# Performance work log

Measured on AMD Instinct MI355X. Metric: run time of the kernel, lower is better.

## Reference

```python
import jax, jax.numpy as jnp
import numpy as np

N, E, FD, H, NG, LAT = 20000, 320000, 64, 4, 64, 512


def _gat(x, W, a_src, a_dst, b, src, dst):
    # x: [N, in]; W: [H*FD, in]; a_src/a_dst: [H, FD]; b: [H*FD]
    h = (x @ W.T).reshape(N, H, FD)
    s = jnp.sum(h * a_src, -1)   # [N, H]
    d = jnp.sum(h * a_dst, -1)   # [N, H]
    e = jax.nn.leaky_relu(s[src] + d[dst], negative_slope=0.2)  # [E', H]
    m = jax.ops.segment_max(e, dst, num_segments=N)
    ex = jnp.exp(e - m[dst])
    den = jax.ops.segment_sum(ex, dst, num_segments=N)
    alpha = ex / den[dst]                                        # [E', H]
    out = jax.ops.segment_sum(alpha[:, :, None] * h[src], dst, num_segments=N)
    return out.reshape(N, H * FD) + b


def setup_inputs() -> dict:
    key = jax.random.key(0)
    ks = jax.random.split(key, 24)
    inp = {}
    inp['street_feature'] = jax.random.normal(ks[0], (N, 128), jnp.float32)
    inp['building_feature'] = jax.random.normal(ks[1], (N, 5), jnp.float32)
    sm = jax.random.randint(ks[2], (N, 1), 0, 2).astype(jnp.float32)
    inp['street_mask'] = sm
    inp['building_mask'] = 1.0 - sm
    inp['edge_index'] = jax.random.randint(ks[3], (2, E), 0, N, dtype=jnp.int32)
    # batch: sorted graph ids covering all NG graphs (no empty segments)
    rest = jax.random.randint(ks[4], (N - NG,), 0, NG, dtype=jnp.int32)
    inp['batch'] = jnp.sort(jnp.concatenate([jnp.arange(NG, dtype=jnp.int32), rest]))

    def lin(k, o, i):
        s = 1.0 / np.sqrt(i)
        return jax.random.uniform(k, (o, i), jnp.float32, -s, s)

    inp['street_W'] = lin(ks[5], FD, 128); inp['street_b'] = jnp.zeros((FD,), jnp.float32)
    inp['building_W'] = lin(ks[6], FD, 5); inp['building_b'] = jnp.zeros((FD,), jnp.float32)
    inp['W1'] = lin(ks[7], H * FD, FD)
    inp['a_src1'] = jax.random.normal(ks[8], (H, FD), jnp.float32) * 0.1
    inp['a_dst1'] = jax.random.normal(ks[9], (H, FD), jnp.float32) * 0.1
    inp['b1'] = jnp.zeros((H * FD,), jnp.float32)
    inp['W2'] = lin(ks[10], H * FD, H * FD)
    inp['a_src2'] = jax.random.normal(ks[11], (H, FD), jnp.float32) * 0.1
    inp['a_dst2'] = jax.random.normal(ks[12], (H, FD), jnp.float32) * 0.1
    inp['b2'] = jnp.zeros((H * FD,), jnp.float32)
    inp['W3'] = lin(ks[13], H * FD, H * FD)
    inp['a_src3'] = jax.random.normal(ks[14], (H, FD), jnp.float32) * 0.1
    inp['a_dst3'] = jax.random.normal(ks[15], (H, FD), jnp.float32) * 0.1
    inp['b3'] = jnp.zeros((H * FD,), jnp.float32)
    agg_in = FD * (1 + H * 3)  # 832
    inp['agg_W'] = lin(ks[16], LAT, agg_in); inp['agg_b'] = jnp.zeros((LAT,), jnp.float32)
    inp['mu_W'] = lin(ks[17], LAT, LAT); inp['mu_b'] = jnp.zeros((LAT,), jnp.float32)
    inp['var_W'] = lin(ks[18], LAT, LAT); inp['var_b'] = jnp.zeros((LAT,), jnp.float32)
    return inp


def reference(street_feature, building_feature, street_mask, building_mask,
              edge_index, batch,
              street_W, street_b, building_W, building_b,
              W1, a_src1, a_dst1, b1, W2, a_src2, a_dst2, b2,
              W3, a_src3, a_dst3, b3, agg_W, agg_b, mu_W, mu_b, var_W, var_b):
    sf = jax.nn.relu(street_feature @ street_W.T + street_b)
    bf = jax.nn.relu(building_feature @ building_W.T + building_b)
    n0 = sf * street_mask + bf * building_mask  # [N, FD]
    # add self loops (PyG GATConv default)
    loop = jnp.arange(N, dtype=edge_index.dtype)
    src = jnp.concatenate([edge_index[0], loop])
    dst = jnp.concatenate([edge_index[1], loop])
    n1 = jax.nn.relu(_gat(n0, W1, a_src1, a_dst1, b1, src, dst))
    n2 = jax.nn.relu(_gat(n1, W2, a_src2, a_dst2, b2, src, dst))
    n3 = jax.nn.relu(_gat(n2, W3, a_src3, a_dst3, b3, src, dst))
    g0 = jax.ops.segment_max(n0, batch, num_segments=NG)
    g1 = jax.ops.segment_max(n1, batch, num_segments=NG)
    g2 = jax.ops.segment_max(n2, batch, num_segments=NG)
    g3 = jax.ops.segment_max(n3, batch, num_segments=NG)
    g = jnp.concatenate([g0, g1, g2, g3], axis=1)  # [NG, FD*(1+3H)]
    latent = g @ agg_W.T + agg_b
    mu = latent @ mu_W.T + mu_b
    log_var = latent @ var_W.T + var_b
    return (mu, log_var)
```

## Files before the change

kernel.cpp:

```cpp
#include <hip/hip_runtime.h>
#include <math.h>

#define NNODES 20000
#define NEDGES 320000
#define FDIM 64
#define NHEAD 4
#define NGR 64
#define LATD 512
#define HF 256
#define NEP (NEDGES + NNODES)
#define AGGIN 832
#define MPAD 20032

typedef float f32x4 __attribute__((ext_vector_type(4)));
typedef _Float16 f16x8 __attribute__((ext_vector_type(8)));
typedef unsigned short u16x8 __attribute__((ext_vector_type(8)));

__device__ inline unsigned short f2h(float f) {
    _Float16 h = (_Float16)f;
    unsigned short u;
    __builtin_memcpy(&u, &h, 2);
    return u;
}
__device__ inline float h2f(unsigned short u) {
    _Float16 h;
    __builtin_memcpy(&h, &u, 2);
    return (float)h;
}

#define EDGE_BLOCKS4 ((NEP + 1023) / 1024)
#define CONV_N (HF * FDIM + 2 * HF * HF)
#define CONV_BLOCKS ((CONV_N + 255) / 256)
#define ENC_BLOCKS (NNODES / 32)
#define GEMM_BLOCKS (NNODES / 32)
#define SLAB_BLOCKS (NNODES / 32)

__global__ void prep_kernel(
    const int* __restrict__ ei, int* __restrict__ cnt,
    const float* __restrict__ W1, const float* __restrict__ W2, const float* __restrict__ W3,
    unsigned short* __restrict__ W1f, unsigned short* __restrict__ W2f,
    unsigned short* __restrict__ W3f)
{
    if (blockIdx.x < EDGE_BLOCKS4) {
        int i0 = blockIdx.x * 1024 + threadIdx.x;
#pragma unroll
        for (int u = 0; u < 4; u++) {
            int i = i0 + u * 256;
            if (i < NEDGES) {
                atomicAdd(&cnt[ei[NEDGES + i]], 1);
            } else if (i < NEP) {
                atomicAdd(&cnt[i - NEDGES], 1);
            }
        }
    } else {
        int i = (blockIdx.x - EDGE_BLOCKS4) * 256 + threadIdx.x;
        const int n1 = HF * FDIM, n2 = HF * HF;
        const float* src; unsigned short* dst; int j;
        if (i < n1) { src = W1; dst = W1f; j = i; }
        else if (i < n1 + n2) { src = W2; dst = W2f; j = i - n1; }
        else if (i < n1 + 2 * n2) { src = W3; dst = W3f; j = i - n1 - n2; }
        else return;
        dst[j] = f2h(src[j]);
    }
}

__global__ __launch_bounds__(1024) void scan_deg(const int* __restrict__ deg, int* __restrict__ offs)
{
    __shared__ int wt[16];
    const int per = (NNODES + 1023) / 1024;
    int t = threadIdx.x, lane = t & 63, w = t >> 6;
    int start = t * per;
    int end = start + per; if (end > NNODES) end = NNODES;
    int s = 0;
    for (int i = start; i < end; i++) s += deg[i];
    int pref = s;
#pragma unroll
    for (int m = 1; m < 64; m <<= 1) {
        int v = __shfl_up(pref, m, 64);
        if (lane >= m) pref += v;
    }
    if (lane == 63) wt[w] = pref;
    __syncthreads();
    int wadd = 0;
    for (int i = 0; i < w; i++) wadd += wt[i];
    int acc = wadd + pref - s;
    for (int i = start; i < end; i++) { offs[i] = acc; acc += deg[i]; }
    if (t == 1023) offs[NNODES] = NEP;
}

__global__ void scatter_edges(const int* __restrict__ ei, const int* __restrict__ offs,
                              int* __restrict__ cnt2, int* __restrict__ csr_src)
{
    int i0 = blockIdx.x * 1024 + threadIdx.x;
    int sv[4], dv[4];
#pragma unroll
    for (int u = 0; u < 4; u++) {
        int i = i0 + u * 256;
        if (i < NEDGES) { sv[u] = ei[i]; dv[u] = ei[NEDGES + i]; }
        else if (i < NEP) { sv[u] = i - NEDGES; dv[u] = i - NEDGES; }
        else { sv[u] = -1; dv[u] = 0; }
    }
#pragma unroll
    for (int u = 0; u < 4; u++) {
        if (sv[u] >= 0) {
            int p = offs[dv[u]] + atomicAdd(&cnt2[dv[u]], 1);
            csr_src[p] = sv[u];
        }
    }
}

__global__ __launch_bounds__(256) void encode_n0(
    const float* __restrict__ sfeat, const float* __restrict__ bfeat,
    const float* __restrict__ smask, const float* __restrict__ bmask,
    const float* __restrict__ sW, const float* __restrict__ sb,
    const float* __restrict__ bW, const float* __restrict__ bb,
    const int* __restrict__ batch,
    unsigned short* __restrict__ x0, int* __restrict__ g)
{
    __shared__ float wlds[64 * 132];
    int t = threadIdx.x;
#pragma unroll
    for (int it = 0; it < 8; it++) {
        int idx = it * 256 + t;
        int f = idx >> 5, k4 = idx & 31;
        float4 v = *(const float4*)(sW + f * 128 + k4 * 4);
        *(float4*)(&wlds[f * 132 + k4 * 4]) = v;
    }
    __syncthreads();

    int lane = t & 63, wave = t >> 6;
    int nb = blockIdx.x * 32 + wave * 8;

    float acc[8];
#pragma unroll
    for (int i = 0; i < 8; i++) acc[i] = 0.f;

    const float* xbase = sfeat + (size_t)nb * 128;
    for (int k4 = 0; k4 < 32; k4++) {
        float4 wv = *(const float4*)(&wlds[lane * 132 + k4 * 4]);
#pragma unroll
        for (int i = 0; i < 8; i++) {
            float4 xv = *(const float4*)(xbase + i * 128 + k4 * 4);
            acc[i] += xv.x * wv.x + xv.y * wv.y + xv.z * wv.z + xv.w * wv.w;
        }
    }

    float bwr[5];
#pragma unroll
    for (int k = 0; k < 5; k++) bwr[k] = bW[lane * 5 + k];
    float sbv = sb[lane], bbv = bb[lane];

    int curb = batch[nb];
    float m = 0.f;
#pragma unroll
    for (int i = 0; i < 8; i++) {
        int node = nb + i;
        float accb = 0.f;
#pragma unroll
        for (int k = 0; k < 5; k++) accb += bfeat[node * 5 + k] * bwr[k];
        float sv = fmaxf(acc[i] + sbv, 0.f);
        float bv = fmaxf(accb + bbv, 0.f);
        float val = sv * smask[node] + bv * bmask[node];
        x0[(size_t)node * FDIM + lane] = f2h(val);
        int b = batch[node];
        if (b != curb) {
            atomicMax(&g[curb * AGGIN + lane], __float_as_int(m));
            m = 0.f; curb = b;
        }
        m = fmaxf(m, val);
    }
    atomicMax(&g[curb * AGGIN + lane], __float_as_int(m));
}

template <int K>
__global__ __launch_bounds__(256, 2) void gemm_attn_mfma(
    const unsigned short* __restrict__ xf, const unsigned short* __restrict__ Wf,
    const float* __restrict__ a_src, const float* __restrict__ a_dst,
    unsigned short* __restrict__ h, float* __restrict__ s, float* __restrict__ d,
    const int* __restrict__ batch, int* __restrict__ g, int slabcol)
{
    if (blockIdx.x >= GEMM_BLOCKS) {
        int f = threadIdx.x;
        int r0 = (blockIdx.x - GEMM_BLOCKS) * 32;
        int cur = batch[r0];
        float m = 0.f;
        for (int r = r0; r < r0 + 32; r += 4) {
            float v[4]; int bb[4];
#pragma unroll
            for (int i = 0; i < 4; i++) {
                v[i] = h2f(xf[(size_t)(r + i) * K + f]);
                bb[i] = batch[r + i];
            }
#pragma unroll
            for (int i = 0; i < 4; i++) {
                if (bb[i] != cur) {
                    atomicMax(&g[cur * AGGIN + slabcol + f], __float_as_int(m));
                    m = 0.f; cur = bb[i];
                }
                m = fmaxf(m, v[i]);
            }
        }
        atomicMax(&g[cur * AGGIN + slabcol + f], __float_as_int(m));
        return;
    }

    constexpr int NCHUNK = K / 64;
    int t = threadIdx.x, lane = t & 63, w = t >> 6;
    int colid = lane & 15, quad = lane >> 4;
    int nb = blockIdx.x * 32;

    f32x4 acc[2][4];
#pragma unroll
    for (int mt = 0; mt < 2; mt++)
#pragma unroll
        for (int nt = 0; nt < 4; nt++)
#pragma unroll
            for (int r = 0; r < 4; r++) acc[mt][nt][r] = 0.f;

#pragma unroll
    for (int c = 0; c < NCHUNK; c++) {
        const int kc = c * 64;
        f16x8 ah[2][2], bh[4][2];
#pragma unroll
        for (int half = 0; half < 2; half++) {
#pragma unroll
            for (int mt = 0; mt < 2; mt++) {
                size_t aoff = (size_t)(nb + mt * 16 + colid) * K + kc + half * 32 + quad * 8;
                ah[mt][half] = *(const f16x8*)&xf[aoff];
            }
#pragma unroll
            for (int nt = 0; nt < 4; nt++) {
                size_t boff = (size_t)(w * 64 + nt * 16 + colid) * K + kc + half * 32 + quad * 8;
                bh[nt][half] = *(const f16x8*)&Wf[boff];
            }
        }
        __builtin_amdgcn_sched_barrier(0);
#pragma unroll
        for (int half = 0; half < 2; half++)
#pragma unroll
            for (int mt = 0; mt < 2; mt++)
#pragma unroll
                for (int nt = 0; nt < 4; nt++)
                    acc[mt][nt] = __builtin_amdgcn_mfma_f32_16x16x32_f16(ah[mt][half], bh[nt][half], acc[mt][nt], 0, 0, 0);
    }

#pragma unroll
    for (int mt = 0; mt < 2; mt++) {
#pragma unroll
        for (int r = 0; r < 4; r++) {
            int node = nb + mt * 16 + quad * 4 + r;
#pragma unroll
            for (int nt = 0; nt < 4; nt++)
                h[(size_t)node * HF + w * 64 + nt * 16 + colid] = f2h(acc[mt][nt][r]);
        }
    }

    float as_r[4], ad_r[4];
#pragma unroll
    for (int nt = 0; nt < 4; nt++) {
        as_r[nt] = a_src[w * 64 + nt * 16 + colid];
        ad_r[nt] = a_dst[w * 64 + nt * 16 + colid];
    }
#pragma unroll
    for (int mt = 0; mt < 2; mt++) {
#pragma unroll
        for (int r = 0; r < 4; r++) {
            float ps = 0.f, pd = 0.f;
#pragma unroll
            for (int nt = 0; nt < 4; nt++) {
                ps += acc[mt][nt][r] * as_r[nt];
                pd += acc[mt][nt][r] * ad_r[nt];
            }
#pragma unroll
            for (int m = 1; m < 16; m <<= 1) {
                ps += __shfl_xor(ps, m, 64);
                pd += __shfl_xor(pd, m, 64);
            }
            if (colid == 0) {
                int node = nb + mt * 16 + quad * 4 + r;
                s[(size_t)node * NHEAD + w] = ps;
                d[(size_t)node * NHEAD + w] = pd;
            }
        }
    }
}

__global__ __launch_bounds__(256) void gat_aggr(
    const unsigned short* __restrict__ h, const float* __restrict__ s, const float* __restrict__ d,
    const int* __restrict__ offs, const int* __restrict__ csr_src,
    const float* __restrict__ bias, unsigned short* __restrict__ out)
{
    int t = threadIdx.x;
    int lane = t & 63;
    int wv = t >> 6;
    int node = blockIdx.x * 4 + wv;
    int eh = lane >> 5;
    int p = lane & 31;
    int hd2 = p >> 3;
    int f0 = p * 8;
    int lo = offs[node], hi = offs[node + 1];
    int deg = hi - lo;

    float a[8];
#pragma unroll
    for (int j = 0; j < 8; j++) a[j] = 0.f;
    float inv;

    if (deg <= 64) {
        int slot = lane >> 2, hd = lane & 3;
        float dn = d[(size_t)node * NHEAD + hd];
        float ev[4];
        int sv[4];
#pragma unroll
        for (int c = 0; c < 4; c++) {
            int k = c * 16 + slot;
            float e = -3.402823466e38f;
            int src = 0;
            if (k < deg) {
                src = csr_src[lo + k];
                float ee = s[(size_t)src * NHEAD + hd] + dn;
                e = fmaxf(ee, 0.2f * ee);
            }
            ev[c] = e; sv[c] = src;
        }
        float mx = fmaxf(fmaxf(ev[0], ev[1]), fmaxf(ev[2], ev[3]));
#pragma unroll
        for (int m = 4; m < 64; m <<= 1) mx = fmaxf(mx, __shfl_xor(mx, m, 64));
        float den = 0.f;
#pragma unroll
        for (int c = 0; c < 4; c++) {
            ev[c] = __expf(ev[c] - mx);
            den += ev[c];
        }
#pragma unroll
        for (int m = 4; m < 64; m <<= 1) den += __shfl_xor(den, m, 64);

        inv = 1.f / __shfl(den, hd2);

#pragma unroll
        for (int cb = 0; cb < 2; cb++) {
            if (cb * 32 >= deg) break;
            float ex[16]; int sr[16]; u16x8 hv[16];
#pragma unroll
            for (int cc = 0; cc < 2; cc++) {
                int c = cb * 2 + cc;
#pragma unroll
                for (int u = 0; u < 8; u++) {
                    int sl = (u * 2 + eh) * 4 + hd2;
                    ex[cc * 8 + u] = __shfl(ev[c], sl);
                    sr[cc * 8 + u] = __shfl(sv[c], sl);
                }
            }
#pragma unroll
            for (int u = 0; u < 16; u++)
                hv[u] = *(const u16x8*)(h + (size_t)sr[u] * HF + f0);
#pragma unroll
            for (int u = 0; u < 16; u++)
#pragma unroll
                for (int j = 0; j < 8; j++) a[j] += ex[u] * h2f(hv[u][j]);
        }
    } else {
        float dn2 = d[(size_t)node * NHEAD + hd2];
        float mx = -3.402823466e38f;
        for (int i = lo; i < hi; i++) {
            int src = csr_src[i];
            float e = s[(size_t)src * NHEAD + hd2] + dn2;
            e = fmaxf(e, 0.2f * e);
            mx = fmaxf(mx, e);
        }
        float den = 0.f;
        for (int i = lo + eh; i < hi; i += 2) {
            int src = csr_src[i];
            float e = s[(size_t)src * NHEAD + hd2] + dn2;
            e = fmaxf(e, 0.2f * e);
            float ex = __expf(e - mx);
            den += ex;
            u16x8 hv = *(const u16x8*)(h + (size_t)src * HF + f0);
#pragma unroll
            for (int j = 0; j < 8; j++) a[j] += ex * h2f(hv[j]);
        }
        den += __shfl_xor(den, 32, 64);
        inv = 1.f / den;
    }

#pragma unroll
    for (int j = 0; j < 8; j++) a[j] += __shfl_xor(a[j], 32, 64);

    if (eh == 0) {
        u16x8 ov;
#pragma unroll
        for (int j = 0; j < 8; j++)
            ov[j] = f2h(fmaxf(a[j] * inv + bias[f0 + j], 0.f));
        *(u16x8*)(out + (size_t)node * HF + f0) = ov;
    }
}

__global__ __launch_bounds__(256) void seg_max_slab_f16(
    const unsigned short* __restrict__ x, const int* __restrict__ batch,
    int* __restrict__ g, int coloff)
{
    int f = threadIdx.x;
    int r0 = blockIdx.x * 32;
    int cur = batch[r0];
    float m = 0.f;
    for (int r = r0; r < r0 + 32; r += 4) {
        float v[4]; int bb[4];
#pragma unroll
        for (int i = 0; i < 4; i++) {
            v[i] = h2f(x[(size_t)(r + i) * HF + f]);
            bb[i] = batch[r + i];
        }
#pragma unroll
        for (int i = 0; i < 4; i++) {
            if (bb[i] != cur) {
                atomicMax(&g[cur * AGGIN + coloff + f], __float_as_int(m));
                m = 0.f; cur = bb[i];
            }
            m = fmaxf(m, v[i]);
        }
    }
    atomicMax(&g[cur * AGGIN + coloff + f], __float_as_int(m));
}

__global__ __launch_bounds__(256) void mlp_latent(
    const float* __restrict__ g, const float* __restrict__ W, const float* __restrict__ b,
    float* __restrict__ latent)
{
    int idx = blockIdx.x * 256 + threadIdx.x;
    int r = idx >> 9, c = idx & 511;
    const float4* gv = (const float4*)(g + (size_t)r * AGGIN);
    const float4* wv = (const float4*)(W + (size_t)c * AGGIN);
    float acc = 0.f;
#pragma unroll 4
    for (int k = 0; k < AGGIN / 4; k++) {
        float4 a = gv[k], w = wv[k];
        acc += a.x * w.x + a.y * w.y + a.z * w.z + a.w * w.w;
    }
    latent[idx] = acc + b[c];
}

__global__ __launch_bounds__(256) void mlp_head(
    const float* __restrict__ latent,
    const float* __restrict__ muW, const float* __restrict__ mub,
    const float* __restrict__ vW, const float* __restrict__ vb,
    float* __restrict__ out)
{
    int idx = blockIdx.x * 256 + threadIdx.x;
    int half = idx >> 15;
    int j = idx & 32767;
    int r = j >> 9, c = j & 511;
    const float* W = half ? vW : muW;
    const float* bb = half ? vb : mub;
    const float4* lv = (const float4*)(latent + (size_t)r * LATD);
    const float4* wv = (const float4*)(W + (size_t)c * LATD);
    float acc = 0.f;
#pragma unroll 4
    for (int k = 0; k < LATD / 4; k++) {
        float4 a = lv[k], w = wv[k];
        acc += a.x * w.x + a.y * w.y + a.z * w.z + a.w * w.w;
    }
    out[idx] = acc + bb[c];
}

static inline size_t align16(size_t x) { return (x + 15) & ~(size_t)15; }

extern "C" void kernel_launch(void* const* d_in, const int* in_sizes, int n_in,
                              void* d_out, int out_size, void* d_ws, size_t ws_size,
                              hipStream_t stream)
{
    const float* sfeat = (const float*)d_in[0];
    const float* bfeat = (const float*)d_in[1];
    const float* smask = (const float*)d_in[2];
    const float* bmask = (const float*)d_in[3];
    const int*   ei    = (const int*)d_in[4];
    const int*   batch = (const int*)d_in[5];
    const float* sW = (const float*)d_in[6];
    const float* sb = (const float*)d_in[7];
    const float* bW = (const float*)d_in[8];
    const float* bb = (const float*)d_in[9];
    const float* W1 = (const float*)d_in[10];
    const float* as1 = (const float*)d_in[11];
    const float* ad1 = (const float*)d_in[12];
    const float* b1 = (const float*)d_in[13];
    const float* W2 = (const float*)d_in[14];
    const float* as2 = (const float*)d_in[15];
    const float* ad2 = (const float*)d_in[16];
    const float* b2 = (const float*)d_in[17];
    const float* W3 = (const float*)d_in[18];
    const float* as3 = (const float*)d_in[19];
    const float* ad3 = (const float*)d_in[20];
    const float* b3 = (const float*)d_in[21];
    const float* aggW = (const float*)d_in[22];
    const float* aggb = (const float*)d_in[23];
    const float* muW = (const float*)d_in[24];
    const float* mub = (const float*)d_in[25];
    const float* vW = (const float*)d_in[26];
    const float* vb = (const float*)d_in[27];
    float* out = (float*)d_out;

    char* ws = (char*)d_ws;
    size_t off = 0;
    unsigned short* h  = (unsigned short*)(ws + off); off = align16(off + (size_t)NNODES * HF * 2);
    unsigned short* x0 = (unsigned short*)(ws + off); off = align16(off + (size_t)MPAD * FDIM * 2);
    unsigned short* xA = (unsigned short*)(ws + off); off = align16(off + (size_t)MPAD * HF * 2);
    float* s  = (float*)(ws + off); off = align16(off + (size_t)NNODES * NHEAD * 4);
    float* d  = (float*)(ws + off); off = align16(off + (size_t)NNODES * NHEAD * 4);
    int* offs = (int*)(ws + off);   off = align16(off + (size_t)(NNODES + 1) * 4);
    size_t zstart = off;
    int* cnt  = (int*)(ws + off);   off = align16(off + (size_t)NNODES * 4);
    int* cnt2 = (int*)(ws + off);   off = align16(off + (size_t)NNODES * 4);
    float* g  = (float*)(ws + off); off = align16(off + (size_t)NGR * AGGIN * 4);
    size_t zbytes = off - zstart;
    int* csr  = (int*)(ws + off);   off = align16(off + (size_t)NEP * 4);
    float* lat = (float*)(ws + off); off = align16(off + (size_t)NGR * LATD * 4);
    unsigned short* W1f = (unsigned short*)(ws + off); off = align16(off + (size_t)HF * FDIM * 2);
    unsigned short* W2f = (unsigned short*)(ws + off); off = align16(off + (size_t)HF * HF * 2);
    unsigned short* W3f = (unsigned short*)(ws + off); off = align16(off + (size_t)HF * HF * 2);

    hipMemsetAsync(ws + zstart, 0, zbytes, stream);

    prep_kernel<<<EDGE_BLOCKS4 + CONV_BLOCKS, 256, 0, stream>>>(
        ei, cnt, W1, W2, W3, W1f, W2f, W3f);
    scan_deg<<<1, 1024, 0, stream>>>(cnt, offs);
    scatter_edges<<<EDGE_BLOCKS4, 256, 0, stream>>>(ei, offs, cnt2, csr);
    encode_n0<<<ENC_BLOCKS, 256, 0, stream>>>(
        sfeat, bfeat, smask, bmask, sW, sb, bW, bb, batch, x0, (int*)g);

    gemm_attn_mfma<FDIM><<<GEMM_BLOCKS, 256, 0, stream>>>(
        x0, W1f, as1, ad1, h, s, d, batch, (int*)g, -1);
    gat_aggr<<<NNODES / 4, 256, 0, stream>>>(h, s, d, offs, csr, b1, xA);

    gemm_attn_mfma<HF><<<GEMM_BLOCKS + SLAB_BLOCKS, 256, 0, stream>>>(
        xA, W2f, as2, ad2, h, s, d, batch, (int*)g, FDIM);
    gat_aggr<<<NNODES / 4, 256, 0, stream>>>(h, s, d, offs, csr, b2, xA);

    gemm_attn_mfma<HF><<<GEMM_BLOCKS + SLAB_BLOCKS, 256, 0, stream>>>(
        xA, W3f, as3, ad3, h, s, d, batch, (int*)g, FDIM + HF);
    gat_aggr<<<NNODES / 4, 256, 0, stream>>>(h, s, d, offs, csr, b3, xA);

    seg_max_slab_f16<<<SLAB_BLOCKS, 256, 0, stream>>>(xA, batch, (int*)g, FDIM + 2 * HF);

    mlp_latent<<<(NGR * LATD + 255) / 256, 256, 0, stream>>>(g, aggW, aggb, lat);
    mlp_head<<<(2 * NGR * LATD + 255) / 256, 256, 0, stream>>>(lat, muW, mub, vW, vb, out);
}
```

Baseline: 386.2 us.

## Fuse whole pipeline into one cooperative persistent kernel with grid syncs

```diff
diff --git a/kernel.cpp b/kernel.cpp
--- a/kernel.cpp
+++ b/kernel.cpp
@@ -1,5 +1,8 @@
 #include <hip/hip_runtime.h>
+#include <hip/hip_cooperative_groups.h>
 #include <math.h>
+
+namespace cg = cooperative_groups;
 
 #define NNODES 20000
 #define NEDGES 320000
@@ -12,104 +15,62 @@
 #define AGGIN 832
 #define MPAD 20032
 
-typedef float f32x4 __attribute__((ext_vector_type(4)));
-typedef _Float16 f16x8 __attribute__((ext_vector_type(8)));
-typedef unsigned short u16x8 __attribute__((ext_vector_type(8)));
-
-__device__ inline unsigned short f2h(float f) {
-    _Float16 h = (_Float16)f;
-    unsigned short u;
-    __builtin_memcpy(&u, &h, 2);
-    return u;
-}
-__device__ inline float h2f(unsigned short u) {
-    _Float16 h;
-    __builtin_memcpy(&h, &u, 2);
-    return (float)h;
-}
-
 #define EDGE_BLOCKS4 ((NEP + 1023) / 1024)
 #define CONV_N (HF * FDIM + 2 * HF * HF)
 #define CONV_BLOCKS ((CONV_N + 255) / 256)
 #define ENC_BLOCKS (NNODES / 32)
 #define GEMM_BLOCKS (NNODES / 32)
 #define SLAB_BLOCKS (NNODES / 32)
-
-__global__ void prep_kernel(
-    const int* __restrict__ ei, int* __restrict__ cnt,
+#define AGGR_BLOCKS (NNODES / 4)
+
+typedef float f32x4 __attribute__((ext_vector_type(4)));
+typedef _Float16 f16x8 __attribute__((ext_vector_type(8)));
+typedef unsigned short u16x8 __attribute__((ext_vector_type(8)));
+
+__device__ inline unsigned short f2h(float f) {
+    _Float16 h = (_Float16)f;
+    unsigned short u;
+    __builtin_memcpy(&u, &h, 2);
+    return u;
+}
+__device__ inline float h2f(unsigned short u) {
+    _Float16 h;
+    __builtin_memcpy(&h, &u, 2);
+    return (float)h;
+}
+
+
+__device__ __forceinline__ void count_body(int vb, int t,
+    const int* __restrict__ ei, int* __restrict__ cnt)
+{
+    int i0 = vb * 1024 + t;
+#pragma unroll
+    for (int u = 0; u < 4; u++) {
+        int i = i0 + u * 256;
+        if (i < NEDGES) {
+            atomicAdd(&cnt[ei[NEDGES + i]], 1);
+        } else if (i < NEP) {
+            atomicAdd(&cnt[i - NEDGES], 1);
+        }
+    }
+}
+
+__device__ __forceinline__ void convert_body(int vb, int t,
     const float* __restrict__ W1, const float* __restrict__ W2, const float* __restrict__ W3,
     unsigned short* __restrict__ W1f, unsigned short* __restrict__ W2f,
     unsigned short* __restrict__ W3f)
 {
-    if (blockIdx.x < EDGE_BLOCKS4) {
-        int i0 = blockIdx.x * 1024 + threadIdx.x;
-#pragma unroll
-        for (int u = 0; u < 4; u++) {
-            int i = i0 + u * 256;
-            if (i < NEDGES) {
-                atomicAdd(&cnt[ei[NEDGES + i]], 1);
-            } else if (i < NEP) {
-                atomicAdd(&cnt[i - NEDGES], 1);
-            }
-        }
-    } else {
-        int i = (blockIdx.x - EDGE_BLOCKS4) * 256 + threadIdx.x;
-        const int n1 = HF * FDIM, n2 = HF * HF;
-        const float* src; unsigned short* dst; int j;
-        if (i < n1) { src = W1; dst = W1f; j = i; }
-        else if (i < n1 + n2) { src = W2; dst = W2f; j = i - n1; }
-        else if (i < n1 + 2 * n2) { src = W3; dst = W3f; j = i - n1 - n2; }
-        else return;
-        dst[j] = f2h(src[j]);
-    }
-}
-
-__global__ __launch_bounds__(1024) void scan_deg(const int* __restrict__ deg, int* __restrict__ offs)
-{
-    __shared__ int wt[16];
-    const int per = (NNODES + 1023) / 1024;
-    int t = threadIdx.x, lane = t & 63, w = t >> 6;
-    int start = t * per;
-    int end = start + per; if (end > NNODES) end = NNODES;
-    int s = 0;
-    for (int i = start; i < end; i++) s += deg[i];
-    int pref = s;
-#pragma unroll
-    for (int m = 1; m < 64; m <<= 1) {
-        int v = __shfl_up(pref, m, 64);
-        if (lane >= m) pref += v;
-    }
-    if (lane == 63) wt[w] = pref;
-    __syncthreads();
-    int wadd = 0;
-    for (int i = 0; i < w; i++) wadd += wt[i];
-    int acc = wadd + pref - s;
-    for (int i = start; i < end; i++) { offs[i] = acc; acc += deg[i]; }
-    if (t == 1023) offs[NNODES] = NEP;
-}
-
-__global__ void scatter_edges(const int* __restrict__ ei, const int* __restrict__ offs,
-                              int* __restrict__ cnt2, int* __restrict__ csr_src)
-{
-    int i0 = blockIdx.x * 1024 + threadIdx.x;
-    int sv[4], dv[4];
-#pragma unroll
-    for (int u = 0; u < 4; u++) {
-        int i = i0 + u * 256;
-        if (i < NEDGES) { sv[u] = ei[i]; dv[u] = ei[NEDGES + i]; }
-        else if (i < NEP) { sv[u] = i - NEDGES; dv[u] = i - NEDGES; }
-        else { sv[u] = -1; dv[u] = 0; }
-    }
-#pragma unroll
-    for (int u = 0; u < 4; u++) {
-        if (sv[u] >= 0) {
-            int p = offs[dv[u]] + atomicAdd(&cnt2[dv[u]], 1);
-            csr_src[p] = sv[u];
-        }
-    }
-}
-
-__global__ __launch_bounds__(256) void encode_n0(
+    int i = vb * 256 + t;
+    const int n1 = HF * FDIM, n2 = HF * HF;
+    const float* src; unsigned short* dst; int j;
+    if (i < n1) { src = W1; dst = W1f; j = i; }
+    else if (i < n1 + n2) { src = W2; dst = W2f; j = i - n1; }
+    else if (i < n1 + 2 * n2) { src = W3; dst = W3f; j = i - n1 - n2; }
+    else return;
+    dst[j] = f2h(src[j]);
+}
+
+__device__ __forceinline__ void encode_body(int venc, int t, bool& wloaded, float* wlds,
     const float* __restrict__ sfeat, const float* __restrict__ bfeat,
     const float* __restrict__ smask, const float* __restrict__ bmask,
     const float* __restrict__ sW, const float* __restrict__ sb,
@@ -117,19 +78,20 @@
     const int* __restrict__ batch,
     unsigned short* __restrict__ x0, int* __restrict__ g)
 {
-    __shared__ float wlds[64 * 132];
-    int t = threadIdx.x;
-#pragma unroll
-    for (int it = 0; it < 8; it++) {
-        int idx = it * 256 + t;
-        int f = idx >> 5, k4 = idx & 31;
-        float4 v = *(const float4*)(sW + f * 128 + k4 * 4);
-        *(float4*)(&wlds[f * 132 + k4 * 4]) = v;
+    if (!wloaded) {
+#pragma unroll
+        for (int it = 0; it < 8; it++) {
+            int idx = it * 256 + t;
+            int f = idx >> 5, k4 = idx & 31;
+            float4 v = *(const float4*)(sW + f * 128 + k4 * 4);
+            *(float4*)(&wlds[f * 132 + k4 * 4]) = v;
+        }
+        wloaded = true;
     }
     __syncthreads();
 
     int lane = t & 63, wave = t >> 6;
-    int nb = blockIdx.x * 32 + wave * 8;
+    int nb = venc * 32 + wave * 8;
 
     float acc[8];
 #pragma unroll
@@ -172,42 +134,62 @@
     atomicMax(&g[curb * AGGIN + lane], __float_as_int(m));
 }
 
+__device__ __forceinline__ void scan_body(int t,
+    const int* __restrict__ deg, int* __restrict__ offs, int* wt)
+{
+    const int per = (NNODES + 255) / 256;
+    int lane = t & 63, w = t >> 6;
+    int start = t * per;
+    int end = start + per; if (end > NNODES) end = NNODES;
+    int s = 0;
+    for (int i = start; i < end; i++) s += deg[i];
+    int pref = s;
+#pragma unroll
+    for (int m = 1; m < 64; m <<= 1) {
+        int v = __shfl_up(pref, m, 64);
+        if (lane >= m) pref += v;
+    }
+    if (lane == 63) wt[w] = pref;
+    __syncthreads();
+    int wadd = 0;
+    for (int i = 0; i < w; i++) wadd += wt[i];
+    int acc = wadd + pref - s;
+    for (int i = start; i < end; i++) { offs[i] = acc; acc += deg[i]; }
+    if (t == 255) offs[NNODES] = NEP;
+}
+
+__device__ __forceinline__ void scatter_body(int vb, int t,
+    const int* __restrict__ ei, const int* __restrict__ offs,
+    int* __restrict__ cnt2, int* __restrict__ csr_src)
+{
+    int i0 = vb * 1024 + t;
+    int sv[4], dv[4];
+#pragma unroll
+    for (int u = 0; u < 4; u++) {
+        int i = i0 + u * 256;
+        if (i < NEDGES) { sv[u] = ei[i]; dv[u] = ei[NEDGES + i]; }
+        else if (i < NEP) { sv[u] = i - NEDGES; dv[u] = i - NEDGES; }
+        else { sv[u] = -1; dv[u] = 0; }
+    }
+#pragma unroll
+    for (int u = 0; u < 4; u++) {
+        if (sv[u] >= 0) {
+            int p = offs[dv[u]] + atomicAdd(&cnt2[dv[u]], 1);
+            csr_src[p] = sv[u];
+        }
+    }
+}
+
 template <int K>
-__global__ __launch_bounds__(256, 2) void gemm_attn_mfma(
+__device__ __forceinline__ void gemm_body(int vbg, int t,
     const unsigned short* __restrict__ xf, const unsigned short* __restrict__ Wf,
     const float* __restrict__ a_src, const float* __restrict__ a_dst,
-    unsigned short* __restrict__ h, float* __restrict__ s, float* __restrict__ d,
-    const int* __restrict__ batch, int* __restrict__ g, int slabcol)
-{
-    if (blockIdx.x >= GEMM_BLOCKS) {
-        int f = threadIdx.x;
-        int r0 = (blockIdx.x - GEMM_BLOCKS) * 32;
-        int cur = batch[r0];
-        float m = 0.f;
-        for (int r = r0; r < r0 + 32; r += 4) {
-            float v[4]; int bb[4];
-#pragma unroll
-            for (int i = 0; i < 4; i++) {
-                v[i] = h2f(xf[(size_t)(r + i) * K + f]);
-                bb[i] = batch[r + i];
-            }
-#pragma unroll
-            for (int i = 0; i < 4; i++) {
-                if (bb[i] != cur) {
-                    atomicMax(&g[cur * AGGIN + slabcol + f], __float_as_int(m));
-                    m = 0.f; cur = bb[i];
-                }
-                m = fmaxf(m, v[i]);
-            }
-        }
-        atomicMax(&g[cur * AGGIN + slabcol + f], __float_as_int(m));
-        return;
-    }
-
+    unsigned short* __restrict__ h, float* __restrict__ s, float* __restrict__ d)
+{
     constexpr int NCHUNK = K / 64;
-    int t = threadIdx.x, lane = t & 63, w = t >> 6;
+    int lane = t & 63, w = t >> 6;
     int colid = lane & 15, quad = lane >> 4;
-    int nb = blockIdx.x * 32;
+    int nb = vbg * 32;
 
     f32x4 acc[2][4];
 #pragma unroll
@@ -285,15 +267,14 @@
     }
 }
 
-__global__ __launch_bounds__(256) void gat_aggr(
+__device__ __forceinline__ void aggr_body(int vba, int t,
     const unsigned short* __restrict__ h, const float* __restrict__ s, const float* __restrict__ d,
     const int* __restrict__ offs, const int* __restrict__ csr_src,
     const float* __restrict__ bias, unsigned short* __restrict__ out)
 {
-    int t = threadIdx.x;
     int lane = t & 63;
     int wv = t >> 6;
-    int node = blockIdx.x * 4 + wv;
+    int node = vba * 4 + wv;
     int eh = lane >> 5;
     int p = lane & 31;
     int hd2 = p >> 3;
@@ -395,12 +376,12 @@
     }
 }
 
-__global__ __launch_bounds__(256) void seg_max_slab_f16(
+__device__ __forceinline__ void slab_body(int vbs, int t,
     const unsigned short* __restrict__ x, const int* __restrict__ batch,
     int* __restrict__ g, int coloff)
 {
-    int f = threadIdx.x;
-    int r0 = blockIdx.x * 32;
+    int f = t;
+    int r0 = vbs * 32;
     int cur = batch[r0];
     float m = 0.f;
     for (int r = r0; r < r0 + 32; r += 4) {
@@ -422,11 +403,11 @@
     atomicMax(&g[cur * AGGIN + coloff + f], __float_as_int(m));
 }
 
-__global__ __launch_bounds__(256) void mlp_latent(
+__device__ __forceinline__ void latent_body(int vb, int t,
     const float* __restrict__ g, const float* __restrict__ W, const float* __restrict__ b,
     float* __restrict__ latent)
 {
-    int idx = blockIdx.x * 256 + threadIdx.x;
+    int idx = vb * 256 + t;
     int r = idx >> 9, c = idx & 511;
     const float4* gv = (const float4*)(g + (size_t)r * AGGIN);
     const float4* wv = (const float4*)(W + (size_t)c * AGGIN);
@@ -439,18 +420,18 @@
     latent[idx] = acc + b[c];
 }
 
-__global__ __launch_bounds__(256) void mlp_head(
+__device__ __forceinline__ void head_body(int vb, int t,
     const float* __restrict__ latent,
     const float* __restrict__ muW, const float* __restrict__ mub,
-    const float* __restrict__ vW, const float* __restrict__ vb,
+    const float* __restrict__ vW, const float* __restrict__ vb_,
     float* __restrict__ out)
 {
-    int idx = blockIdx.x * 256 + threadIdx.x;
+    int idx = vb * 256 + t;
     int half = idx >> 15;
     int j = idx & 32767;
     int r = j >> 9, c = j & 511;
     const float* W = half ? vW : muW;
-    const float* bb = half ? vb : mub;
+    const float* bb = half ? vb_ : mub;
     const float4* lv = (const float4*)(latent + (size_t)r * LATD);
     const float4* wv = (const float4*)(W + (size_t)c * LATD);
     float acc = 0.f;
@@ -462,84 +443,255 @@
     out[idx] = acc + bb[c];
 }
 
+struct MegaParams {
+    const float *sfeat, *bfeat, *smask, *bmask;
+    const int *ei, *batch;
+    const float *sW, *sb, *bW, *bb;
+    const float *W1, *as1, *ad1, *b1;
+    const float *W2, *as2, *ad2, *b2;
+    const float *W3, *as3, *ad3, *b3;
+    const float *aggW, *aggb, *muW, *mub, *vW, *varb;
+    float *out;
+    unsigned short *h, *x0, *xA, *W1f, *W2f, *W3f;
+    float *s, *d, *g, *lat;
+    int *offs, *cnt, *cnt2, *csr, *gi;
+};
+
+__global__ __launch_bounds__(256, 2) void mega(MegaParams P)
+{
+    cg::grid_group grid = cg::this_grid();
+    __shared__ float wlds[64 * 132];
+    __shared__ int wt[4];
+    const int t = threadIdx.x;
+    const int bid = blockIdx.x;
+    const int G = gridDim.x;
+    bool wloaded = false;
+
+    for (int vb = bid; vb < EDGE_BLOCKS4 + CONV_BLOCKS + ENC_BLOCKS; vb += G) {
+        if (vb < EDGE_BLOCKS4)
+            count_body(vb, t, P.ei, P.cnt);
+        else if (vb < EDGE_BLOCKS4 + CONV_BLOCKS)
+            convert_body(vb - EDGE_BLOCKS4, t, P.W1, P.W2, P.W3, P.W1f, P.W2f, P.W3f);
+        else
+            encode_body(vb - (EDGE_BLOCKS4 + CONV_BLOCKS), t, wloaded, wlds,
+                        P.sfeat, P.bfeat, P.smask, P.bmask, P.sW, P.sb, P.bW, P.bb,
+                        P.batch, P.x0, P.gi);
+    }
+    grid.sync();
+
+    if (bid == G - 1) {
+        scan_body(t, P.cnt, P.offs, wt);
+    } else {
+        for (int vb = bid; vb < GEMM_BLOCKS; vb += G - 1)
+            gemm_body<FDIM>(vb, t, P.x0, P.W1f, P.as1, P.ad1, P.h, P.s, P.d);
+    }
+    grid.sync();
+
+    for (int vb = bid; vb < EDGE_BLOCKS4; vb += G)
+        scatter_body(vb, t, P.ei, P.offs, P.cnt2, P.csr);
+    grid.sync();
+
+    for (int vb = bid; vb < AGGR_BLOCKS; vb += G)
+        aggr_body(vb, t, P.h, P.s, P.d, P.offs, P.csr, P.b1, P.xA);
+    grid.sync();
+
+    for (int vb = bid; vb < GEMM_BLOCKS + SLAB_BLOCKS; vb += G) {
+        if (vb < GEMM_BLOCKS)
+            gemm_body<HF>(vb, t, P.xA, P.W2f, P.as2, P.ad2, P.h, P.s, P.d);
+        else
+            slab_body(vb - GEMM_BLOCKS, t, P.xA, P.batch, P.gi, FDIM);
+    }
+    grid.sync();
+
+    for (int vb = bid; vb < AGGR_BLOCKS; vb += G)
+        aggr_body(vb, t, P.h, P.s, P.d, P.offs, P.csr, P.b2, P.xA);
+    grid.sync();
+
+    for (int vb = bid; vb < GEMM_BLOCKS + SLAB_BLOCKS; vb += G) {
+        if (vb < GEMM_BLOCKS)
+            gemm_body<HF>(vb, t, P.xA, P.W3f, P.as3, P.ad3, P.h, P.s, P.d);
+        else
+            slab_body(vb - GEMM_BLOCKS, t, P.xA, P.batch, P.gi, FDIM + HF);
+    }
+    grid.sync();
+
+    for (int vb = bid; vb < AGGR_BLOCKS; vb += G)
+        aggr_body(vb, t, P.h, P.s, P.d, P.offs, P.csr, P.b3, P.xA);
+    grid.sync();
+
+    for (int vb = bid; vb < SLAB_BLOCKS; vb += G)
+        slab_body(vb, t, P.xA, P.batch, P.gi, FDIM + 2 * HF);
+    grid.sync();
+
+    for (int vb = bid; vb < (NGR * LATD) / 256; vb += G)
+        latent_body(vb, t, P.g, P.aggW, P.aggb, P.lat);
+    grid.sync();
+
+    for (int vb = bid; vb < (2 * NGR * LATD) / 256; vb += G)
+        head_body(vb, t, P.lat, P.muW, P.mub, P.vW, P.varb, P.out);
+}
+
+__global__ __launch_bounds__(256) void k_prep(MegaParams P)
+{
+    if ((int)blockIdx.x < EDGE_BLOCKS4)
+        count_body(blockIdx.x, threadIdx.x, P.ei, P.cnt);
+    else
+        convert_body(blockIdx.x - EDGE_BLOCKS4, threadIdx.x, P.W1, P.W2, P.W3,
+                     P.W1f, P.W2f, P.W3f);
+}
+
+__global__ __launch_bounds__(256) void k_scan(MegaParams P)
+{
+    __shared__ int wt[4];
+    scan_body(threadIdx.x, P.cnt, P.offs, wt);
+}
+
+__global__ __launch_bounds__(256) void k_scatter_encode(MegaParams P)
+{
+    __shared__ float wlds[64 * 132];
+    bool wloaded = false;
+    if ((int)blockIdx.x < EDGE_BLOCKS4)
+        scatter_body(blockIdx.x, threadIdx.x, P.ei, P.offs, P.cnt2, P.csr);
+    else
+        encode_body(blockIdx.x - EDGE_BLOCKS4, threadIdx.x, wloaded, wlds,
+                    P.sfeat, P.bfeat, P.smask, P.bmask, P.sW, P.sb, P.bW, P.bb,
+                    P.batch, P.x0, P.gi);
+}
+
+template <int K>
+__global__ __launch_bounds__(256, 2) void k_gemm(MegaParams P,
+    const unsigned short* xf, const unsigned short* Wf,
+    const float* a_src, const float* a_dst, int slabcol)
+{
+    if ((int)blockIdx.x >= GEMM_BLOCKS) {
+        slab_body(blockIdx.x - GEMM_BLOCKS, threadIdx.x, xf, P.batch, P.gi, slabcol);
+        return;
+    }
+    gemm_body<K>(blockIdx.x, threadIdx.x, xf, Wf, a_src, a_dst, P.h, P.s, P.d);
+}
+
+__global__ __launch_bounds__(256) void k_aggr(MegaParams P, const float* bias)
+{
+    aggr_body(blockIdx.x, threadIdx.x, P.h, P.s, P.d, P.offs, P.csr, bias, P.xA);
+}
+
+__global__ __launch_bounds__(256) void k_slab(MegaParams P, int coloff)
+{
+    slab_body(blockIdx.x, threadIdx.x, P.xA, P.batch, P.gi, coloff);
+}
+
+__global__ __launch_bounds__(256) void k_latent(MegaParams P)
+{
+    latent_body(blockIdx.x, threadIdx.x, P.g, P.aggW, P.aggb, P.lat);
+}
+
+__global__ __launch_bounds__(256) void k_head(MegaParams P)
+{
+    head_body(blockIdx.x, threadIdx.x, P.lat, P.muW, P.mub, P.vW, P.varb, P.out);
+}
+
 static inline size_t align16(size_t x) { return (x + 15) & ~(size_t)15; }
 
 extern "C" void kernel_launch(void* const* d_in, const int* in_sizes, int n_in,
                               void* d_out, int out_size, void* d_ws, size_t ws_size,
                               hipStream_t stream)
 {
-    const float* sfeat = (const float*)d_in[0];
-    const float* bfeat = (const float*)d_in[1];
-    const float* smask = (const float*)d_in[2];
-    const float* bmask = (const float*)d_in[3];
-    const int*   ei    = (const int*)d_in[4];
-    const int*   batch = (const int*)d_in[5];
-    const float* sW = (const float*)d_in[6];
-    const float* sb = (const float*)d_in[7];
-    const float* bW = (const float*)d_in[8];
-    const float* bb = (const float*)d_in[9];
-    const float* W1 = (const float*)d_in[10];
-    const float* as1 = (const float*)d_in[11];
-    const float* ad1 = (const float*)d_in[12];
-    const float* b1 = (const float*)d_in[13];
-    const float* W2 = (const float*)d_in[14];
-    const float* as2 = (const float*)d_in[15];
-    const float* ad2 = (const float*)d_in[16];
-    const float* b2 = (const float*)d_in[17];
-    const float* W3 = (const float*)d_in[18];
-    const float* as3 = (const float*)d_in[19];
-    const float* ad3 = (const float*)d_in[20];
-    const float* b3 = (const float*)d_in[21];
-    const float* aggW = (const float*)d_in[22];
-    const float* aggb = (const float*)d_in[23];
-    const float* muW = (const float*)d_in[24];
-    const float* mub = (const float*)d_in[25];
-    const float* vW = (const float*)d_in[26];
-    const float* vb = (const float*)d_in[27];
-    float* out = (float*)d_out;
+    MegaParams P;
+    P.sfeat = (const float*)d_in[0];
+    P.bfeat = (const float*)d_in[1];
+    P.smask = (const float*)d_in[2];
+    P.bmask = (const float*)d_in[3];
+    P.ei    = (const int*)d_in[4];
+    P.batch = (const int*)d_in[5];
+    P.sW = (const float*)d_in[6];
+    P.sb = (const float*)d_in[7];
+    P.bW = (const float*)d_in[8];
+    P.bb = (const float*)d_in[9];
+    P.W1 = (const float*)d_in[10];
+    P.as1 = (const float*)d_in[11];
+    P.ad1 = (const float*)d_in[12];
+    P.b1 = (const float*)d_in[13];
+    P.W2 = (const float*)d_in[14];
+    P.as2 = (const float*)d_in[15];
+    P.ad2 = (const float*)d_in[16];
+    P.b2 = (const float*)d_in[17];
+    P.W3 = (const float*)d_in[18];
+    P.as3 = (const float*)d_in[19];
+    P.ad3 = (const float*)d_in[20];
+    P.b3 = (const float*)d_in[21];
+    P.aggW = (const float*)d_in[22];
+    P.aggb = (const float*)d_in[23];
+    P.muW = (const float*)d_in[24];
+    P.mub = (const float*)d_in[25];
+    P.vW = (const float*)d_in[26];
+    P.varb = (const float*)d_in[27];
+    P.out = (float*)d_out;
 
     char* ws = (char*)d_ws;
     size_t off = 0;
-    unsigned short* h  = (unsigned short*)(ws + off); off = align16(off + (size_t)NNODES * HF * 2);
-    unsigned short* x0 = (unsigned short*)(ws + off); off = align16(off + (size_t)MPAD * FDIM * 2);
-    unsigned short* xA = (unsigned short*)(ws + off); off = align16(off + (size_t)MPAD * HF * 2);
-    float* s  = (float*)(ws + off); off = align16(off + (size_t)NNODES * NHEAD * 4);
-    float* d  = (float*)(ws + off); off = align16(off + (size_t)NNODES * NHEAD * 4);
-    int* offs = (int*)(ws + off);   off = align16(off + (size_t)(NNODES + 1) * 4);
+    P.h  = (unsigned short*)(ws + off); off = align16(off + (size_t)NNODES * HF * 2);
+    P.x0 = (unsigned short*)(ws + off); off = align16(off + (size_t)MPAD * FDIM * 2);
+    P.xA = (unsigned short*)(ws + off); off = align16(off + (size_t)MPAD * HF * 2);
+    P.s  = (float*)(ws + off); off = align16(off + (size_t)NNODES * NHEAD * 4);
+    P.d  = (float*)(ws + off); off = align16(off + (size_t)NNODES * NHEAD * 4);
+    P.offs = (int*)(ws + off); off = align16(off + (size_t)(NNODES + 1) * 4);
     size_t zstart = off;
-    int* cnt  = (int*)(ws + off);   off = align16(off + (size_t)NNODES * 4);
-    int* cnt2 = (int*)(ws + off);   off = align16(off + (size_t)NNODES * 4);
-    float* g  = (float*)(ws + off); off = align16(off + (size_t)NGR * AGGIN * 4);
+    P.cnt  = (int*)(ws + off); off = align16(off + (size_t)NNODES * 4);
+    P.cnt2 = (int*)(ws + off); off = align16(off + (size_t)NNODES * 4);
+    P.g    = (float*)(ws + off); off = align16(off + (size_t)NGR * AGGIN * 4);
     size_t zbytes = off - zstart;
-    int* csr  = (int*)(ws + off);   off = align16(off + (size_t)NEP * 4);
-    float* lat = (float*)(ws + off); off = align16(off + (size_t)NGR * LATD * 4);
-    unsigned short* W1f = (unsigned short*)(ws + off); off = align16(off + (size_t)HF * FDIM * 2);
-    unsigned short* W2f = (unsigned short*)(ws + off); off = align16(off + (size_t)HF * HF * 2);
-    unsigned short* W3f = (unsigned short*)(ws + off); off = align16(off + (size_t)HF * HF * 2);
+    P.csr = (int*)(ws + off); off = align16(off + (size_t)NEP * 4);
+    P.lat = (float*)(ws + off); off = align16(off + (size_t)NGR * LATD * 4);
+    P.W1f = (unsigned short*)(ws + off); off = align16(off + (size_t)HF * FDIM * 2);
+    P.W2f = (unsigned short*)(ws + off); off = align16(off + (size_t)HF * HF * 2);
+    P.W3f = (unsigned short*)(ws + off); off = align16(off + (size_t)HF * HF * 2);
+
+    P.gi = (int*)P.g;
 
     hipMemsetAsync(ws + zstart, 0, zbytes, stream);
 
-    prep_kernel<<<EDGE_BLOCKS4 + CONV_BLOCKS, 256, 0, stream>>>(
-        ei, cnt, W1, W2, W3, W1f, W2f, W3f);
-    scan_deg<<<1, 1024, 0, stream>>>(cnt, offs);
-    scatter_edges<<<EDGE_BLOCKS4, 256, 0, stream>>>(ei, offs, cnt2, csr);
-    encode_n0<<<ENC_BLOCKS, 256, 0, stream>>>(
-        sfeat, bfeat, smask, bmask, sW, sb, bW, bb, batch, x0, (int*)g);
-
-    gemm_attn_mfma<FDIM><<<GEMM_BLOCKS, 256, 0, stream>>>(
-        x0, W1f, as1, ad1, h, s, d, batch, (int*)g, -1);
-    gat_aggr<<<NNODES / 4, 256, 0, stream>>>(h, s, d, offs, csr, b1, xA);
-
-    gemm_attn_mfma<HF><<<GEMM_BLOCKS + SLAB_BLOCKS, 256, 0, stream>>>(
-        xA, W2f, as2, ad2, h, s, d, batch, (int*)g, FDIM);
-    gat_aggr<<<NNODES / 4, 256, 0, stream>>>(h, s, d, offs, csr, b2, xA);
-
-    gemm_attn_mfma<HF><<<GEMM_BLOCKS + SLAB_BLOCKS, 256, 0, stream>>>(
-        xA, W3f, as3, ad3, h, s, d, batch, (int*)g, FDIM + HF);
-    gat_aggr<<<NNODES / 4, 256, 0, stream>>>(h, s, d, offs, csr, b3, xA);
-
-    seg_max_slab_f16<<<SLAB_BLOCKS, 256, 0, stream>>>(xA, batch, (int*)g, FDIM + 2 * HF);
-
-    mlp_latent<<<(NGR * LATD + 255) / 256, 256, 0, stream>>>(g, aggW, aggb, lat);
-    mlp_head<<<(2 * NGR * LATD + 255) / 256, 256, 0, stream>>>(lat, muW, mub, vW, vb, out);
-}
+    static int s_maxb = -2;
+    static int s_mp = 256;
+    if (s_maxb == -2) {
+        int dev = 0;
+        hipGetDevice(&dev);
+        hipDeviceProp_t prop;
+        if (hipGetDeviceProperties(&prop, dev) == hipSuccess && prop.multiProcessorCount > 0)
+            s_mp = prop.multiProcessorCount;
+        int mb = 0;
+        if (hipOccupancyMaxActiveBlocksPerMultiprocessor(&mb, mega, 256, 0) != hipSuccess)
+            mb = 0;
+        s_maxb = mb;
+    }
+
+    bool coop_ok = false;
+    if (s_maxb >= 1) {
+        int grid = s_maxb * s_mp;
+        if (grid > 1024) grid = 1024;
+        if (grid >= 2) {
+            void* kargs[] = { (void*)&P };
+            coop_ok = (hipLaunchCooperativeKernel(reinterpret_cast<const void*>(mega),
+                                                  dim3(grid), dim3(256), kargs, 0,
+                                                  stream) == hipSuccess);
+        }
+    }
+
+    if (!coop_ok) {
+        k_prep<<<EDGE_BLOCKS4 + CONV_BLOCKS, 256, 0, stream>>>(P);
+        k_scan<<<1, 256, 0, stream>>>(P);
+        k_scatter_encode<<<EDGE_BLOCKS4 + ENC_BLOCKS, 256, 0, stream>>>(P);
+
+        k_gemm<FDIM><<<GEMM_BLOCKS, 256, 0, stream>>>(P, P.x0, P.W1f, P.as1, P.ad1, -1);
+        k_aggr<<<AGGR_BLOCKS, 256, 0, stream>>>(P, P.b1);
+
+        k_gemm<HF><<<GEMM_BLOCKS + SLAB_BLOCKS, 256, 0, stream>>>(P, P.xA, P.W2f, P.as2, P.ad2, FDIM);
+        k_aggr<<<AGGR_BLOCKS, 256, 0, stream>>>(P, P.b2);
+
+        k_gemm<HF><<<GEMM_BLOCKS + SLAB_BLOCKS, 256, 0, stream>>>(P, P.xA, P.W3f, P.as3, P.ad3, FDIM + HF);
+        k_aggr<<<AGGR_BLOCKS, 256, 0, stream>>>(P, P.b3);
+
+        k_slab<<<SLAB_BLOCKS, 256, 0, stream>>>(P, FDIM + 2 * HF);
+        k_latent<<<(NGR * LATD) / 256, 256, 0, stream>>>(P);
+        k_head<<<(2 * NGR * LATD) / 256, 256, 0, stream>>>(P);
+    }
+}
```

Result: slower. 804.1 us (+108.2%).
